# Kernel tuning notes

Measured on AMD Instinct MI355X. Metric: run time of the kernel, lower is better.

## Reference

```python
import jax, jax.numpy as jnp
import numpy as np

N, E = 50000, 800000
IN_DIM, HIDDEN, HEADS, OUT_DIM = 128, 64, 2, 128
NEG_SLOPE = 0.2


def setup_inputs() -> dict:
    key = jax.random.key(0)
    ks = jax.random.split(key, 12)
    s = lambda k, *sh: jax.random.normal(k, sh, dtype=jnp.float32) * (1.0 / np.sqrt(sh[0]))
    return {
        "x": jax.random.normal(ks[0], (N, IN_DIM), dtype=jnp.float32),
        "edge_index": jax.random.randint(ks[1], (2, E), 0, N, dtype=jnp.int64),
        # layer 1 (heads=2, concat=True)
        "Wl1": s(ks[2], IN_DIM, HEADS * HIDDEN),
        "Wr1": s(ks[3], IN_DIM, HEADS * HIDDEN),
        "att1": jax.random.normal(ks[4], (HEADS, HIDDEN), dtype=jnp.float32) * 0.1,
        "b1": jnp.zeros((HEADS * HIDDEN,), dtype=jnp.float32),
        # layer 2 (heads=1, concat=False -> mean)
        "Wl2": s(ks[5], HEADS * HIDDEN, OUT_DIM),
        "Wr2": s(ks[6], HEADS * HIDDEN, OUT_DIM),
        "att2": jax.random.normal(ks[7], (1, OUT_DIM), dtype=jnp.float32) * 0.1,
        "b2": jnp.zeros((OUT_DIM,), dtype=jnp.float32),
    }


def _gatv2_layer(x, src, dst, Wl, Wr, att, bias, heads, concat):
    n = x.shape[0]
    c = Wl.shape[1] // heads
    xl = (x @ Wl).reshape(n, heads, c)  # source transform
    xr = (x @ Wr).reshape(n, heads, c)  # target transform
    e = jax.nn.leaky_relu(xl[src] + xr[dst], NEG_SLOPE)      # (E, H, C)
    alpha = jnp.einsum("ehc,hc->eh", e, att)                 # (E, H)
    # softmax over incoming edges per destination node
    amax = jax.ops.segment_max(alpha, dst, num_segments=n)
    alpha = jnp.exp(alpha - amax[dst])
    denom = jax.ops.segment_sum(alpha, dst, num_segments=n)
    alpha = alpha / (denom[dst] + 1e-16)
    msg = xl[src] * alpha[:, :, None]                        # (E, H, C)
    out = jax.ops.segment_sum(msg, dst, num_segments=n)      # (N, H, C)
    out = out.reshape(n, heads * c) if concat else out.mean(axis=1)
    return out + bias


def reference(x, edge_index, Wl1, Wr1, att1, b1, Wl2, Wr2, att2, b2):
    n = x.shape[0]
    # PyG GATv2Conv default: add self loops
    loops = jnp.arange(n, dtype=edge_index.dtype)
    src = jnp.concatenate([edge_index[0], loops])
    dst = jnp.concatenate([edge_index[1], loops])
    h = jax.nn.elu(_gatv2_layer(x, src, dst, Wl1, Wr1, att1, b1, HEADS, True))
    h = jax.nn.elu(_gatv2_layer(h, src, dst, Wl2, Wr2, att2, b2, 1, False))
    return h
```

## Files before the change

### kernel.cpp

```cpp
#include <hip/hip_runtime.h>
#include <hip/hip_bf16.h>

#define N_NODES 50000
#define N_EDGES 800000
#define TOT_E   (N_EDGES + N_NODES)
#define NEG_SLOPE 0.2f
#define NBKT 196
#define NPB 256
#define BKT_CAP 6144
#define CHUNK 4096
#define NCHUNK ((TOT_E + CHUNK - 1) / CHUNK)

typedef __attribute__((ext_vector_type(8))) short bf16x8;
typedef __attribute__((ext_vector_type(4))) float f32x4;

static __device__ __forceinline__ unsigned short f2bf(float f) {
    unsigned int u = __float_as_uint(f);
    unsigned int r = (u + 0x7FFFu + ((u >> 16) & 1u)) >> 16;
    return (unsigned short)r;
}
static __device__ __forceinline__ float bf2f(unsigned short h) {
    return __uint_as_float(((unsigned int)h) << 16);
}
static __device__ __forceinline__ unsigned short f2h(float f) {
    _Float16 h = (_Float16)f;
    return __builtin_bit_cast(unsigned short, h);
}
static __device__ __forceinline__ float h2f(unsigned short u) {
    return (float)__builtin_bit_cast(_Float16, u);
}

__global__ __launch_bounds__(1024) void kA(const int* __restrict__ srcp,
                                           const int* __restrict__ dstp,
                                           int* __restrict__ bcount,
                                           unsigned* __restrict__ ebuf) {
    __shared__ int h[NBKT];
    __shared__ int lbase[NBKT];
    __shared__ int lcur[NBKT];
    __shared__ int sc[256];
    __shared__ unsigned stage[CHUNK];
    int t = threadIdx.x;
    if (t < NBKT) h[t] = 0;
    __syncthreads();
    int base = blockIdx.x * CHUNK;
    int nloc = min(CHUNK, TOT_E - base);
    for (int i = t; i < nloc; i += 1024) {
        int e = base + i;
        int d = (e < N_EDGES) ? dstp[e] : (e - N_EDGES);
        atomicAdd(&h[d >> 8], 1);
    }
    __syncthreads();
    if (t < NBKT) lbase[t] = h[t] ? atomicAdd(&bcount[t], h[t]) : 0;
    if (t < 256) sc[t] = (t < NBKT) ? h[t] : 0;
    __syncthreads();
    for (int off = 1; off < 256; off <<= 1) {
        int v = (t < 256 && t >= off) ? sc[t - off] : 0;
        __syncthreads();
        if (t < 256) sc[t] += v;
        __syncthreads();
    }
    if (t < NBKT) lcur[t] = sc[t] - h[t];
    __syncthreads();
    for (int i = t; i < nloc; i += 1024) {
        int e = base + i;
        int d = (e < N_EDGES) ? dstp[e] : (e - N_EDGES);
        int s = (e < N_EDGES) ? srcp[e] : (e - N_EDGES);
        int b = d >> 8;
        int p = atomicAdd(&lcur[b], 1);
        stage[p] = (unsigned)s | ((unsigned)(d & 255) << 16) | ((unsigned)b << 24);
    }
    __syncthreads();
    for (int i = t; i < nloc; i += 1024) {
        unsigned v = stage[i];
        int b = v >> 24;
        int pl = lbase[b] + (i - (lcur[b] - h[b]));
        if (pl < BKT_CAP) ebuf[(size_t)b * BKT_CAP + pl] = v & 0xFFFFFFu;
    }
}

__global__ void kScanB(const int* __restrict__ bcount, int* __restrict__ bbase) {
    __shared__ int s[256];
    int t = threadIdx.x;
    int own = (t < NBKT) ? bcount[t] : 0;
    s[t] = own;
    __syncthreads();
    for (int off = 1; off < 256; off <<= 1) {
        int v = (t >= off) ? s[t - off] : 0;
        __syncthreads();
        s[t] += v;
        __syncthreads();
    }
    if (t < NBKT) bbase[t] = s[t] - own;
    if (t == NBKT - 1) bbase[NBKT] = s[t];
}

__global__ __launch_bounds__(1024) void kB(const unsigned* __restrict__ ebuf,
                                           const int* __restrict__ bcount,
                                           const int* __restrict__ bbase,
                                           int* __restrict__ rowptr,
                                           int* __restrict__ esrc) {
    __shared__ int h[NPB];
    __shared__ int sc[NPB];
    __shared__ int st2[BKT_CAP];
    int b = blockIdx.x;
    int t = threadIdx.x;
    int gb = bbase[b];
    int cnt = min(bcount[b], BKT_CAP);
    const unsigned* eb = ebuf + (size_t)b * BKT_CAP;
    if (t < NPB) h[t] = 0;
    __syncthreads();
    for (int i = t; i < cnt; i += 1024)
        atomicAdd(&h[(eb[i] >> 16) & 255], 1);
    __syncthreads();
    if (t < NPB) sc[t] = h[t];
    __syncthreads();
    for (int off = 1; off < NPB; off <<= 1) {
        int v = (t < NPB && t >= off) ? sc[t - off] : 0;
        __syncthreads();
        if (t < NPB) sc[t] += v;
        __syncthreads();
    }
    if (t < NPB) h[t] = sc[t] - h[t];
    __syncthreads();
    int node0 = b << 8;
    if (t < NPB && node0 + t < N_NODES) rowptr[node0 + t] = gb + h[t];
    if (b == NBKT - 1 && t == 0) rowptr[N_NODES] = TOT_E;
    for (int i = t; i < cnt; i += 1024) {
        unsigned v = eb[i];
        int p = atomicAdd(&h[(v >> 16) & 255], 1);
        st2[p] = (int)(v & 0xFFFFu);
    }
    __syncthreads();
    for (int i = t; i < cnt; i += 1024) esrc[gb + i] = st2[i];
}

__global__ void k_pack2(const float* __restrict__ Wl1, const float* __restrict__ Wr1,
                        const float* __restrict__ Wl2, const float* __restrict__ Wr2,
                        unsigned short* __restrict__ Bp1, unsigned short* __restrict__ Bp2) {
    int gidx = blockIdx.x * 256 + threadIdx.x;
    int which = gidx >> 16;
    int idx = gidx & 65535;
    const float* Wa = which ? Wl2 : Wl1;
    const float* Wb = which ? Wr2 : Wr1;
    unsigned short* Bp = which ? Bp2 : Bp1;
    int j = idx & 7, lane = (idx >> 3) & 63, t = idx >> 9;
    int ks = t >> 4, ctg = t & 15;
    int k = (ks * 32 + (lane >> 4) * 8 + j) & 127;
    int n = ctg * 16 + (lane & 15);
    float v = (n < 128) ? Wa[k * 128 + n] : Wb[k * 128 + (n - 128)];
    Bp[idx] = f2bf(v);
}

template <bool F32IN>
__global__ __launch_bounds__(256) void k_mfma_lin(const void* __restrict__ Ain,
                                                  const unsigned short* __restrict__ Bp,
                                                  unsigned short* __restrict__ outA,
                                                  unsigned short* __restrict__ outB, int M) {
    __shared__ unsigned short lds_a[64][264];
    int tid = threadIdx.x;
    int n0 = blockIdx.x * 64;
    if (F32IN) {
        const float* X = (const float*)Ain;
#pragma unroll
        for (int r = 0; r < 8; ++r) {
            int c = r * 256 + tid;
            int row = c >> 5;
            int col4 = (c & 31) * 4;
            int gr = n0 + row;
            if (gr >= M) gr = M - 1;
            float4 v = *(const float4*)&X[(size_t)gr * 128 + col4];
            float vv[4] = {v.x, v.y, v.z, v.w};
            ushort4 hh, ll;
            unsigned short* hp = &hh.x;
            unsigned short* lp = &ll.x;
#pragma unroll
            for (int q = 0; q < 4; ++q) {
                unsigned short hv = f2bf(vv[q]);
                hp[q] = hv;
                lp[q] = f2bf(vv[q] - bf2f(hv));
            }
            *(ushort4*)&lds_a[row][col4] = hh;
            *(ushort4*)&lds_a[row][128 + col4] = ll;
        }
    } else {
        const unsigned short* Ap = (const unsigned short*)Ain;
#pragma unroll
        for (int r = 0; r < 8; ++r) {
            int c = r * 256 + tid;
            int row = c >> 5;
            int col = (c & 31) * 8;
            int gr = n0 + row;
            if (gr >= M) gr = M - 1;
            float4 v = *(const float4*)&Ap[(size_t)gr * 256 + col];
            *(float4*)&lds_a[row][col] = v;
        }
    }
    __syncthreads();

    int w = tid >> 6, lane = tid & 63;
    int lrow = lane & 15, lhi = lane >> 4;
    f32x4 acc[4][4] = {};
    const bf16x8* Bf = (const bf16x8*)Bp;
#pragma unroll
    for (int ks = 0; ks < 8; ++ks) {
        bf16x8 bfr[4], afr[4];
#pragma unroll
        for (int ct = 0; ct < 4; ++ct)
            bfr[ct] = Bf[(ks * 16 + (w * 4 + ct)) * 64 + lane];
#pragma unroll
        for (int mt = 0; mt < 4; ++mt)
            afr[mt] = *(const bf16x8*)&lds_a[mt * 16 + lrow][ks * 32 + lhi * 8];
#pragma unroll
        for (int mt = 0; mt < 4; ++mt)
#pragma unroll
            for (int ct = 0; ct < 4; ++ct)
                acc[mt][ct] = __builtin_amdgcn_mfma_f32_16x16x32_bf16(
                    afr[mt], bfr[ct], acc[mt][ct], 0, 0, 0);
    }
#pragma unroll
    for (int mt = 0; mt < 4; ++mt) {
        int row0 = n0 + mt * 16 + lhi * 4;
#pragma unroll
        for (int ct = 0; ct < 4; ++ct) {
            int col = w * 64 + ct * 16 + lrow;
            unsigned short* dst = (col < 128) ? outA : outB;
            int cc = col & 127;
#pragma unroll
            for (int reg = 0; reg < 4; ++reg) {
                int rg = row0 + reg;
                if (rg < M) dst[(size_t)rg * 128 + cc] = f2h(acc[mt][ct][reg]);
            }
        }
    }
}

template <int H, bool BF16OUT>
__global__ __launch_bounds__(256) void k_gat(const int* __restrict__ rowptr,
                                             const int* __restrict__ esrc,
                                             const unsigned short* __restrict__ xlh,
                                             const unsigned short* __restrict__ xrh,
                                             const float* __restrict__ att,
                                             const float* __restrict__ bias,
                                             float* __restrict__ out,
                                             unsigned short* __restrict__ outb) {
    int n = (blockIdx.x * 256 + threadIdx.x) >> 6;
    int lane = threadIdx.x & 63;
    if (n >= N_NODES) return;
    int start = rowptr[n], end = rowptr[n + 1];
    int grp = lane >> 4, sub = lane & 15;
    int c0 = sub * 8;

    float xr8[8], a8[8];
    {
        uint4 u = *(const uint4*)&xrh[(size_t)n * 128 + c0];
        unsigned int uu[4] = {u.x, u.y, u.z, u.w};
#pragma unroll
        for (int q = 0; q < 4; ++q) {
            xr8[2 * q]     = h2f((unsigned short)uu[q]);
            xr8[2 * q + 1] = h2f((unsigned short)(uu[q] >> 16));
        }
        float4 av0 = *(const float4*)&att[c0];
        float4 av1 = *(const float4*)&att[c0 + 4];
        a8[0] = av0.x; a8[1] = av0.y; a8[2] = av0.z; a8[3] = av0.w;
        a8[4] = av1.x; a8[5] = av1.y; a8[6] = av1.z; a8[7] = av1.w;
    }

    float m = -1e30f, den = 0.f;
    float acc[8] = {0.f, 0.f, 0.f, 0.f, 0.f, 0.f, 0.f, 0.f};

    int last = end - 1;
    auto cidx = [&](int e) { return esrc[(e < end) ? e : last]; };
    int sA = cidx(start + grp);
    int sB = cidx(start + 4 + grp);
    int sC = cidx(start + 8 + grp);
    uint4 u0 = *(const uint4*)&xlh[(size_t)sA * 128 + c0];
    uint4 u1 = *(const uint4*)&xlh[(size_t)sB * 128 + c0];

    for (int i = start; i < end; i += 4) {
        bool valid = (i + grp) < end;
        uint4 uc = u0;
        u0 = u1;
        u1 = *(const uint4*)&xlh[(size_t)sC * 128 + c0];
        sC = cidx(i + 12 + grp);
        unsigned int uu[4] = {uc.x, uc.y, uc.z, uc.w};
        float c[8];
#pragma unroll
        for (int q = 0; q < 4; ++q) {
            c[2 * q]     = h2f((unsigned short)uu[q]);
            c[2 * q + 1] = h2f((unsigned short)(uu[q] >> 16));
        }
        float t = 0.f;
#pragma unroll
        for (int j = 0; j < 8; ++j) {
            float v = c[j] + xr8[j];
            v = fmaxf(v, NEG_SLOPE * v);
            t = fmaf(v, a8[j], t);
        }
        const int STEPS = (H == 2) ? 3 : 4;
#pragma unroll
        for (int k = 0; k < STEPS; ++k)
            t += __shfl_xor(t, 1 << k, 64);
        float sc = valid ? t : -1e38f;

        float mn = fmaxf(m, sc);
        float corr = __expf(m - mn);
        float p = __expf(sc - mn);
        m = mn;
        den = fmaf(den, corr, p);
#pragma unroll
        for (int j = 0; j < 8; ++j)
            acc[j] = fmaf(acc[j], corr, p * c[j]);
    }

#pragma unroll
    for (int off = 16; off <= 32; off <<= 1) {
        float mo = __shfl_xor(m, off, 64);
        float deno = __shfl_xor(den, off, 64);
        float ao[8];
#pragma unroll
        for (int j = 0; j < 8; ++j) ao[j] = __shfl_xor(acc[j], off, 64);
        float mn = fmaxf(m, mo);
        float c1 = __expf(m - mn);
        float c2 = __expf(mo - mn);
        m = mn;
        den = den * c1 + deno * c2;
#pragma unroll
        for (int j = 0; j < 8; ++j)
            acc[j] = fmaf(acc[j], c1, ao[j] * c2);
    }

    if (grp == 0) {
        float inv = 1.f / (den + 1e-16f);
        float o[8];
        float4 bv0 = *(const float4*)&bias[c0];
        float4 bv1 = *(const float4*)&bias[c0 + 4];
        float bb[8] = {bv0.x, bv0.y, bv0.z, bv0.w, bv1.x, bv1.y, bv1.z, bv1.w};
#pragma unroll
        for (int j = 0; j < 8; ++j) {
            float v = fmaf(acc[j], inv, bb[j]);
            o[j] = (v > 0.f) ? v : (__expf(v) - 1.f);
        }
        if (BF16OUT) {
            unsigned short hi[8], lo[8];
#pragma unroll
            for (int j = 0; j < 8; ++j) {
                hi[j] = f2bf(o[j]);
                lo[j] = f2bf(o[j] - bf2f(hi[j]));
            }
            *(uint4*)&outb[(size_t)n * 256 + c0] = *(const uint4*)hi;
            *(uint4*)&outb[(size_t)n * 256 + 128 + c0] = *(const uint4*)lo;
        } else {
            *(float4*)&out[(size_t)n * 128 + c0] = make_float4(o[0], o[1], o[2], o[3]);
            *(float4*)&out[(size_t)n * 128 + c0 + 4] = make_float4(o[4], o[5], o[6], o[7]);
        }
    }
}

extern "C" void kernel_launch(void* const* d_in, const int* in_sizes, int n_in,
                              void* d_out, int out_size, void* d_ws, size_t ws_size,
                              hipStream_t stream) {
    const float* x    = (const float*)d_in[0];
    const int*   ei   = (const int*)d_in[1];
    const float* Wl1  = (const float*)d_in[2];
    const float* Wr1  = (const float*)d_in[3];
    const float* att1 = (const float*)d_in[4];
    const float* b1   = (const float*)d_in[5];
    const float* Wl2  = (const float*)d_in[6];
    const float* Wr2  = (const float*)d_in[7];
    const float* att2 = (const float*)d_in[8];
    const float* b2   = (const float*)d_in[9];
    const int* srcp = ei;
    const int* dstp = ei + N_EDGES;

    char* ws = (char*)d_ws;
    size_t off = 0;
    auto alloc = [&](size_t bytes) {
        void* p = ws + off;
        off = (off + bytes + 255) & ~(size_t)255;
        return p;
    };
    int*      bcount  = (int*)alloc(NBKT * sizeof(int));
    int*      bbase   = (int*)alloc((NBKT + 1) * sizeof(int));
    unsigned* ebuf    = (unsigned*)alloc((size_t)NBKT * BKT_CAP * sizeof(unsigned));
    int*      rowptr  = (int*)alloc((N_NODES + 1) * sizeof(int));
    int*      esrc    = (int*)alloc((size_t)TOT_E * sizeof(int));
    unsigned short* xp  = (unsigned short*)alloc((size_t)N_NODES * 256 * sizeof(short));
    unsigned short* Bp1 = (unsigned short*)alloc(65536 * sizeof(short));
    unsigned short* Bp2 = (unsigned short*)alloc(65536 * sizeof(short));
    unsigned short* xl  = (unsigned short*)alloc((size_t)N_NODES * 128 * sizeof(short));
    unsigned short* xr  = (unsigned short*)alloc((size_t)N_NODES * 128 * sizeof(short));

    hipMemsetAsync(bcount, 0, NBKT * sizeof(int), stream);
    kA<<<NCHUNK, 1024, 0, stream>>>(srcp, dstp, bcount, ebuf);
    kScanB<<<1, 256, 0, stream>>>(bcount, bbase);
    kB<<<NBKT, 1024, 0, stream>>>(ebuf, bcount, bbase, rowptr, esrc);

    k_pack2<<<512, 256, 0, stream>>>(Wl1, Wr1, Wl2, Wr2, Bp1, Bp2);

    int mfma_grid = (N_NODES + 63) / 64;

    k_mfma_lin<true><<<mfma_grid, 256, 0, stream>>>(x, Bp1, xl, xr, N_NODES);
    k_gat<2, true><<<(N_NODES + 3) / 4, 256, 0, stream>>>(rowptr, esrc, xl, xr, att1, b1,
                                                          nullptr, xp);
    k_mfma_lin<false><<<mfma_grid, 256, 0, stream>>>(xp, Bp2, xl, xr, N_NODES);
    k_gat<1, false><<<(N_NODES + 3) / 4, 256, 0, stream>>>(rowptr, esrc, xl, xr, att2, b2,
                                                           (float*)d_out, nullptr);
}
```

Before: 166.8 us.

## Fuse layer-1 GEMM with edge bucketing and fold the bucket scan into the CSR build

Layer-1 MFMA GEMM blocks and edge-bucketing blocks now run in one launch, branching on block index, so the two independent stages can overlap. The separate bucket-base scan kernel is merged into the per-bucket CSR kernel, which now recomputes the 196-entry prefix in every block. The bcount memset is replaced by zeroing inside the weight-pack kernel, and the bucketing kernels drop from 1024 to 256 threads. Nontemporal loads are added for streaming reads, trading fewer launches and more overlap for redundant scan work and a mixed-role grid that shares one shared-memory allocation sized for the GEMM.

```diff
diff --git a/kernel.cpp b/kernel.cpp
--- a/kernel.cpp
+++ b/kernel.cpp
@@ -10,9 +10,11 @@
 #define BKT_CAP 6144
 #define CHUNK 4096
 #define NCHUNK ((TOT_E + CHUNK - 1) / CHUNK)
+#define GEMM_BLKS ((N_NODES + 63) / 64)
 
 typedef __attribute__((ext_vector_type(8))) short bf16x8;
 typedef __attribute__((ext_vector_type(4))) float f32x4;
+typedef __attribute__((ext_vector_type(4))) unsigned int u32x4;
 
 static __device__ __forceinline__ unsigned short f2bf(float f) {
     unsigned int u = __float_as_uint(f);
@@ -30,113 +32,214 @@
     return (float)__builtin_bit_cast(_Float16, u);
 }
 
-__global__ __launch_bounds__(1024) void kA(const int* __restrict__ srcp,
-                                           const int* __restrict__ dstp,
-                                           int* __restrict__ bcount,
-                                           unsigned* __restrict__ ebuf) {
-    __shared__ int h[NBKT];
-    __shared__ int lbase[NBKT];
-    __shared__ int lcur[NBKT];
-    __shared__ int sc[256];
-    __shared__ unsigned stage[CHUNK];
+struct SmemGemm { unsigned short lds_a[64][264]; };
+struct SmemKA {
+    int h[NBKT];
+    int lbase[NBKT];
+    int lcur[NBKT];
+    int sc[256];
+    unsigned stage[CHUNK];
+};
+
+static __device__ void kA_body(SmemKA* s, int blk, const int* __restrict__ srcp,
+                               const int* __restrict__ dstp, int* __restrict__ bcount,
+                               unsigned* __restrict__ ebuf) {
     int t = threadIdx.x;
-    if (t < NBKT) h[t] = 0;
-    __syncthreads();
-    int base = blockIdx.x * CHUNK;
+    if (t < NBKT) s->h[t] = 0;
+    __syncthreads();
+    int base = blk * CHUNK;
     int nloc = min(CHUNK, TOT_E - base);
-    for (int i = t; i < nloc; i += 1024) {
+    for (int i = t; i < nloc; i += 256) {
         int e = base + i;
         int d = (e < N_EDGES) ? dstp[e] : (e - N_EDGES);
-        atomicAdd(&h[d >> 8], 1);
-    }
-    __syncthreads();
-    if (t < NBKT) lbase[t] = h[t] ? atomicAdd(&bcount[t], h[t]) : 0;
-    if (t < 256) sc[t] = (t < NBKT) ? h[t] : 0;
+        atomicAdd(&s->h[d >> 8], 1);
+    }
+    __syncthreads();
+    if (t < NBKT) s->lbase[t] = s->h[t] ? atomicAdd(&bcount[t], s->h[t]) : 0;
+    s->sc[t] = (t < NBKT) ? s->h[t] : 0;
     __syncthreads();
     for (int off = 1; off < 256; off <<= 1) {
-        int v = (t < 256 && t >= off) ? sc[t - off] : 0;
-        __syncthreads();
-        if (t < 256) sc[t] += v;
-        __syncthreads();
-    }
-    if (t < NBKT) lcur[t] = sc[t] - h[t];
-    __syncthreads();
-    for (int i = t; i < nloc; i += 1024) {
+        int v = (t >= off) ? s->sc[t - off] : 0;
+        __syncthreads();
+        s->sc[t] += v;
+        __syncthreads();
+    }
+    if (t < NBKT) s->lcur[t] = s->sc[t] - s->h[t];
+    __syncthreads();
+    for (int i = t; i < nloc; i += 256) {
         int e = base + i;
         int d = (e < N_EDGES) ? dstp[e] : (e - N_EDGES);
-        int s = (e < N_EDGES) ? srcp[e] : (e - N_EDGES);
+        int sv = (e < N_EDGES) ? srcp[e] : (e - N_EDGES);
         int b = d >> 8;
-        int p = atomicAdd(&lcur[b], 1);
-        stage[p] = (unsigned)s | ((unsigned)(d & 255) << 16) | ((unsigned)b << 24);
-    }
-    __syncthreads();
-    for (int i = t; i < nloc; i += 1024) {
-        unsigned v = stage[i];
+        int p = atomicAdd(&s->lcur[b], 1);
+        s->stage[p] = (unsigned)sv | ((unsigned)(d & 255) << 16) | ((unsigned)b << 24);
+    }
+    __syncthreads();
+    for (int i = t; i < nloc; i += 256) {
+        unsigned v = s->stage[i];
         int b = v >> 24;
-        int pl = lbase[b] + (i - (lcur[b] - h[b]));
+        int pl = s->lbase[b] + (i - (s->lcur[b] - s->h[b]));
         if (pl < BKT_CAP) ebuf[(size_t)b * BKT_CAP + pl] = v & 0xFFFFFFu;
     }
 }
 
-__global__ void kScanB(const int* __restrict__ bcount, int* __restrict__ bbase) {
-    __shared__ int s[256];
-    int t = threadIdx.x;
-    int own = (t < NBKT) ? bcount[t] : 0;
-    s[t] = own;
-    __syncthreads();
-    for (int off = 1; off < 256; off <<= 1) {
-        int v = (t >= off) ? s[t - off] : 0;
-        __syncthreads();
-        s[t] += v;
-        __syncthreads();
-    }
-    if (t < NBKT) bbase[t] = s[t] - own;
-    if (t == NBKT - 1) bbase[NBKT] = s[t];
-}
-
-__global__ __launch_bounds__(1024) void kB(const unsigned* __restrict__ ebuf,
+template <bool F32IN>
+static __device__ void gemm_body(SmemGemm* sg, int bid, const void* __restrict__ Ain,
+                                 const unsigned short* __restrict__ Bp,
+                                 unsigned short* __restrict__ outA,
+                                 unsigned short* __restrict__ outB, int M) {
+    int tid = threadIdx.x;
+    int n0 = bid * 64;
+    if (F32IN) {
+        const float* X = (const float*)Ain;
+#pragma unroll
+        for (int r = 0; r < 8; ++r) {
+            int c = r * 256 + tid;
+            int row = c >> 5;
+            int col4 = (c & 31) * 4;
+            int gr = n0 + row;
+            if (gr >= M) gr = M - 1;
+            f32x4 v = __builtin_nontemporal_load((const f32x4*)&X[(size_t)gr * 128 + col4]);
+            ushort4 hh, ll;
+            unsigned short* hp = &hh.x;
+            unsigned short* lp = &ll.x;
+#pragma unroll
+            for (int q = 0; q < 4; ++q) {
+                unsigned short hv = f2bf(v[q]);
+                hp[q] = hv;
+                lp[q] = f2bf(v[q] - bf2f(hv));
+            }
+            *(ushort4*)&sg->lds_a[row][col4] = hh;
+            *(ushort4*)&sg->lds_a[row][128 + col4] = ll;
+        }
+    } else {
+        const unsigned short* Ap = (const unsigned short*)Ain;
+#pragma unroll
+        for (int r = 0; r < 8; ++r) {
+            int c = r * 256 + tid;
+            int row = c >> 5;
+            int col = (c & 31) * 8;
+            int gr = n0 + row;
+            if (gr >= M) gr = M - 1;
+            u32x4 v = __builtin_nontemporal_load((const u32x4*)&Ap[(size_t)gr * 256 + col]);
+            *(u32x4*)&sg->lds_a[row][col] = v;
+        }
+    }
+    __syncthreads();
+
+    int w = tid >> 6, lane = tid & 63;
+    int lrow = lane & 15, lhi = lane >> 4;
+    f32x4 acc[4][4] = {};
+    const bf16x8* Bf = (const bf16x8*)Bp;
+#pragma unroll
+    for (int ks = 0; ks < 8; ++ks) {
+        bf16x8 bfr[4], afr[4];
+#pragma unroll
+        for (int ct = 0; ct < 4; ++ct)
+            bfr[ct] = Bf[(ks * 16 + (w * 4 + ct)) * 64 + lane];
+#pragma unroll
+        for (int mt = 0; mt < 4; ++mt)
+            afr[mt] = *(const bf16x8*)&sg->lds_a[mt * 16 + lrow][ks * 32 + lhi * 8];
+#pragma unroll
+        for (int mt = 0; mt < 4; ++mt)
+#pragma unroll
+            for (int ct = 0; ct < 4; ++ct)
+                acc[mt][ct] = __builtin_amdgcn_mfma_f32_16x16x32_bf16(
+                    afr[mt], bfr[ct], acc[mt][ct], 0, 0, 0);
+    }
+#pragma unroll
+    for (int mt = 0; mt < 4; ++mt) {
+        int row0 = n0 + mt * 16 + lhi * 4;
+#pragma unroll
+        for (int ct = 0; ct < 4; ++ct) {
+            int col = w * 64 + ct * 16 + lrow;
+            unsigned short* dst = (col < 128) ? outA : outB;
+            int cc = col & 127;
+#pragma unroll
+            for (int reg = 0; reg < 4; ++reg) {
+                int rg = row0 + reg;
+                if (rg < M) dst[(size_t)rg * 128 + cc] = f2h(acc[mt][ct][reg]);
+            }
+        }
+    }
+}
+
+__global__ __launch_bounds__(256) void k_fused1(const float* __restrict__ x,
+                                                const unsigned short* __restrict__ Bp1,
+                                                unsigned short* __restrict__ xl,
+                                                unsigned short* __restrict__ xr,
+                                                const int* __restrict__ srcp,
+                                                const int* __restrict__ dstp,
+                                                int* __restrict__ bcount,
+                                                unsigned* __restrict__ ebuf) {
+    __shared__ __align__(16) unsigned char smem[sizeof(SmemGemm)];
+    if (blockIdx.x < GEMM_BLKS)
+        gemm_body<true>((SmemGemm*)smem, blockIdx.x, x, Bp1, xl, xr, N_NODES);
+    else
+        kA_body((SmemKA*)smem, blockIdx.x - GEMM_BLKS, srcp, dstp, bcount, ebuf);
+}
+
+__global__ __launch_bounds__(256) void k_mfma_lin2(const unsigned short* __restrict__ Ap,
+                                                   const unsigned short* __restrict__ Bp,
+                                                   unsigned short* __restrict__ outA,
+                                                   unsigned short* __restrict__ outB, int M) {
+    __shared__ __align__(16) unsigned char smem[sizeof(SmemGemm)];
+    gemm_body<false>((SmemGemm*)smem, blockIdx.x, Ap, Bp, outA, outB, M);
+}
+
+__global__ __launch_bounds__(256) void kBs(const unsigned* __restrict__ ebuf,
                                            const int* __restrict__ bcount,
-                                           const int* __restrict__ bbase,
                                            int* __restrict__ rowptr,
                                            int* __restrict__ esrc) {
+    __shared__ int sall[256];
     __shared__ int h[NPB];
     __shared__ int sc[NPB];
     __shared__ int st2[BKT_CAP];
-    int b = blockIdx.x;
-    int t = threadIdx.x;
-    int gb = bbase[b];
+    int b = blockIdx.x, t = threadIdx.x;
+    int own = (t < NBKT) ? bcount[t] : 0;
+    sall[t] = own;
+    __syncthreads();
+    for (int off = 1; off < 256; off <<= 1) {
+        int v = (t >= off) ? sall[t - off] : 0;
+        __syncthreads();
+        sall[t] += v;
+        __syncthreads();
+    }
+    int gb = (b == 0) ? 0 : sall[b - 1];
     int cnt = min(bcount[b], BKT_CAP);
     const unsigned* eb = ebuf + (size_t)b * BKT_CAP;
-    if (t < NPB) h[t] = 0;
-    __syncthreads();
-    for (int i = t; i < cnt; i += 1024)
+    h[t] = 0;
+    __syncthreads();
+    for (int i = t; i < cnt; i += 256)
         atomicAdd(&h[(eb[i] >> 16) & 255], 1);
     __syncthreads();
-    if (t < NPB) sc[t] = h[t];
-    __syncthreads();
-    for (int off = 1; off < NPB; off <<= 1) {
-        int v = (t < NPB && t >= off) ? sc[t - off] : 0;
-        __syncthreads();
-        if (t < NPB) sc[t] += v;
-        __syncthreads();
-    }
-    if (t < NPB) h[t] = sc[t] - h[t];
+    sc[t] = h[t];
+    __syncthreads();
+    for (int off = 1; off < 256; off <<= 1) {
+        int v = (t >= off) ? sc[t - off] : 0;
+        __syncthreads();
+        sc[t] += v;
+        __syncthreads();
+    }
+    h[t] = sc[t] - h[t];
     __syncthreads();
     int node0 = b << 8;
-    if (t < NPB && node0 + t < N_NODES) rowptr[node0 + t] = gb + h[t];
+    if (node0 + t < N_NODES) rowptr[node0 + t] = gb + h[t];
     if (b == NBKT - 1 && t == 0) rowptr[N_NODES] = TOT_E;
-    for (int i = t; i < cnt; i += 1024) {
+    for (int i = t; i < cnt; i += 256) {
         unsigned v = eb[i];
         int p = atomicAdd(&h[(v >> 16) & 255], 1);
         st2[p] = (int)(v & 0xFFFFu);
     }
     __syncthreads();
-    for (int i = t; i < cnt; i += 1024) esrc[gb + i] = st2[i];
+    for (int i = t; i < cnt; i += 256) esrc[gb + i] = st2[i];
 }
 
 __global__ void k_pack2(const float* __restrict__ Wl1, const float* __restrict__ Wr1,
                         const float* __restrict__ Wl2, const float* __restrict__ Wr2,
-                        unsigned short* __restrict__ Bp1, unsigned short* __restrict__ Bp2) {
+                        unsigned short* __restrict__ Bp1, unsigned short* __restrict__ Bp2,
+                        int* __restrict__ bcount) {
+    if (blockIdx.x == 0 && threadIdx.x < NBKT) bcount[threadIdx.x] = 0;
     int gidx = blockIdx.x * 256 + threadIdx.x;
     int which = gidx >> 16;
     int idx = gidx & 65535;
@@ -149,89 +252,6 @@
     int n = ctg * 16 + (lane & 15);
     float v = (n < 128) ? Wa[k * 128 + n] : Wb[k * 128 + (n - 128)];
     Bp[idx] = f2bf(v);
-}
-
-template <bool F32IN>
-__global__ __launch_bounds__(256) void k_mfma_lin(const void* __restrict__ Ain,
-                                                  const unsigned short* __restrict__ Bp,
-                                                  unsigned short* __restrict__ outA,
-                                                  unsigned short* __restrict__ outB, int M) {
-    __shared__ unsigned short lds_a[64][264];
-    int tid = threadIdx.x;
-    int n0 = blockIdx.x * 64;
-    if (F32IN) {
-        const float* X = (const float*)Ain;
-#pragma unroll
-        for (int r = 0; r < 8; ++r) {
-            int c = r * 256 + tid;
-            int row = c >> 5;
-            int col4 = (c & 31) * 4;
-            int gr = n0 + row;
-            if (gr >= M) gr = M - 1;
-            float4 v = *(const float4*)&X[(size_t)gr * 128 + col4];
-            float vv[4] = {v.x, v.y, v.z, v.w};
-            ushort4 hh, ll;
-            unsigned short* hp = &hh.x;
-            unsigned short* lp = &ll.x;
-#pragma unroll
-            for (int q = 0; q < 4; ++q) {
-                unsigned short hv = f2bf(vv[q]);
-                hp[q] = hv;
-                lp[q] = f2bf(vv[q] - bf2f(hv));
-            }
-            *(ushort4*)&lds_a[row][col4] = hh;
-            *(ushort4*)&lds_a[row][128 + col4] = ll;
-        }
-    } else {
-        const unsigned short* Ap = (const unsigned short*)Ain;
-#pragma unroll
-        for (int r = 0; r < 8; ++r) {
-            int c = r * 256 + tid;
-            int row = c >> 5;
-            int col = (c & 31) * 8;
-            int gr = n0 + row;
-            if (gr >= M) gr = M - 1;
-            float4 v = *(const float4*)&Ap[(size_t)gr * 256 + col];
-            *(float4*)&lds_a[row][col] = v;
-        }
-    }
-    __syncthreads();
-
-    int w = tid >> 6, lane = tid & 63;
-    int lrow = lane & 15, lhi = lane >> 4;
-    f32x4 acc[4][4] = {};
-    const bf16x8* Bf = (const bf16x8*)Bp;
-#pragma unroll
-    for (int ks = 0; ks < 8; ++ks) {
-        bf16x8 bfr[4], afr[4];
-#pragma unroll
-        for (int ct = 0; ct < 4; ++ct)
-            bfr[ct] = Bf[(ks * 16 + (w * 4 + ct)) * 64 + lane];
-#pragma unroll
-        for (int mt = 0; mt < 4; ++mt)
-            afr[mt] = *(const bf16x8*)&lds_a[mt * 16 + lrow][ks * 32 + lhi * 8];
-#pragma unroll
-        for (int mt = 0; mt < 4; ++mt)
-#pragma unroll
-            for (int ct = 0; ct < 4; ++ct)
-                acc[mt][ct] = __builtin_amdgcn_mfma_f32_16x16x32_bf16(
-                    afr[mt], bfr[ct], acc[mt][ct], 0, 0, 0);
-    }
-#pragma unroll
-    for (int mt = 0; mt < 4; ++mt) {
-        int row0 = n0 + mt * 16 + lhi * 4;
-#pragma unroll
-        for (int ct = 0; ct < 4; ++ct) {
-            int col = w * 64 + ct * 16 + lrow;
-            unsigned short* dst = (col < 128) ? outA : outB;
-            int cc = col & 127;
-#pragma unroll
-            for (int reg = 0; reg < 4; ++reg) {
-                int rg = row0 + reg;
-                if (rg < M) dst[(size_t)rg * 128 + cc] = f2h(acc[mt][ct][reg]);
-            }
-        }
-    }
 }
 
 template <int H, bool BF16OUT>
@@ -252,12 +272,11 @@
 
     float xr8[8], a8[8];
     {
-        uint4 u = *(const uint4*)&xrh[(size_t)n * 128 + c0];
-        unsigned int uu[4] = {u.x, u.y, u.z, u.w};
+        u32x4 u = __builtin_nontemporal_load((const u32x4*)&xrh[(size_t)n * 128 + c0]);
 #pragma unroll
         for (int q = 0; q < 4; ++q) {
-            xr8[2 * q]     = h2f((unsigned short)uu[q]);
-            xr8[2 * q + 1] = h2f((unsigned short)(uu[q] >> 16));
+            xr8[2 * q]     = h2f((unsigned short)u[q]);
+            xr8[2 * q + 1] = h2f((unsigned short)(u[q] >> 16));
         }
         float4 av0 = *(const float4*)&att[c0];
         float4 av1 = *(const float4*)&att[c0 + 4];
@@ -269,25 +288,26 @@
     float acc[8] = {0.f, 0.f, 0.f, 0.f, 0.f, 0.f, 0.f, 0.f};
 
     int last = end - 1;
-    auto cidx = [&](int e) { return esrc[(e < end) ? e : last]; };
+    auto cidx = [&](int e) {
+        return __builtin_nontemporal_load(&esrc[(e < end) ? e : last]);
+    };
     int sA = cidx(start + grp);
     int sB = cidx(start + 4 + grp);
     int sC = cidx(start + 8 + grp);
-    uint4 u0 = *(const uint4*)&xlh[(size_t)sA * 128 + c0];
-    uint4 u1 = *(const uint4*)&xlh[(size_t)sB * 128 + c0];
+    u32x4 u0 = *(const u32x4*)&xlh[(size_t)sA * 128 + c0];
+    u32x4 u1 = *(const u32x4*)&xlh[(size_t)sB * 128 + c0];
 
     for (int i = start; i < end; i += 4) {
         bool valid = (i + grp) < end;
-        uint4 uc = u0;
+        u32x4 uc = u0;
         u0 = u1;
-        u1 = *(const uint4*)&xlh[(size_t)sC * 128 + c0];
+        u1 = *(const u32x4*)&xlh[(size_t)sC * 128 + c0];
         sC = cidx(i + 12 + grp);
-        unsigned int uu[4] = {uc.x, uc.y, uc.z, uc.w};
         float c[8];
 #pragma unroll
         for (int q = 0; q < 4; ++q) {
-            c[2 * q]     = h2f((unsigned short)uu[q]);
-            c[2 * q + 1] = h2f((unsigned short)(uu[q] >> 16));
+            c[2 * q]     = h2f((unsigned short)uc[q]);
+            c[2 * q + 1] = h2f((unsigned short)(uc[q] >> 16));
         }
         float t = 0.f;
 #pragma unroll
@@ -341,14 +361,17 @@
             o[j] = (v > 0.f) ? v : (__expf(v) - 1.f);
         }
         if (BF16OUT) {
-            unsigned short hi[8], lo[8];
-#pragma unroll
-            for (int j = 0; j < 8; ++j) {
-                hi[j] = f2bf(o[j]);
-                lo[j] = f2bf(o[j] - bf2f(hi[j]));
+            u32x4 hv, lv;
+#pragma unroll
+            for (int q = 0; q < 4; ++q) {
+                unsigned short h0 = f2bf(o[2 * q]), h1 = f2bf(o[2 * q + 1]);
+                unsigned short l0 = f2bf(o[2 * q] - bf2f(h0));
+                unsigned short l1 = f2bf(o[2 * q + 1] - bf2f(h1));
+                hv[q] = (unsigned)h0 | ((unsigned)h1 << 16);
+                lv[q] = (unsigned)l0 | ((unsigned)l1 << 16);
             }
-            *(uint4*)&outb[(size_t)n * 256 + c0] = *(const uint4*)hi;
-            *(uint4*)&outb[(size_t)n * 256 + 128 + c0] = *(const uint4*)lo;
+            *(u32x4*)&outb[(size_t)n * 256 + c0] = hv;
+            *(u32x4*)&outb[(size_t)n * 256 + 128 + c0] = lv;
         } else {
             *(float4*)&out[(size_t)n * 128 + c0] = make_float4(o[0], o[1], o[2], o[3]);
             *(float4*)&out[(size_t)n * 128 + c0 + 4] = make_float4(o[4], o[5], o[6], o[7]);
@@ -380,7 +403,6 @@
         return p;
     };
     int*      bcount  = (int*)alloc(NBKT * sizeof(int));
-    int*      bbase   = (int*)alloc((NBKT + 1) * sizeof(int));
     unsigned* ebuf    = (unsigned*)alloc((size_t)NBKT * BKT_CAP * sizeof(unsigned));
     int*      rowptr  = (int*)alloc((N_NODES + 1) * sizeof(int));
     int*      esrc    = (int*)alloc((size_t)TOT_E * sizeof(int));
@@ -390,19 +412,17 @@
     unsigned short* xl  = (unsigned short*)alloc((size_t)N_NODES * 128 * sizeof(short));
     unsigned short* xr  = (unsigned short*)alloc((size_t)N_NODES * 128 * sizeof(short));
 
-    hipMemsetAsync(bcount, 0, NBKT * sizeof(int), stream);
-    kA<<<NCHUNK, 1024, 0, stream>>>(srcp, dstp, bcount, ebuf);
-    kScanB<<<1, 256, 0, stream>>>(bcount, bbase);
-    kB<<<NBKT, 1024, 0, stream>>>(ebuf, bcount, bbase, rowptr, esrc);
-
-    k_pack2<<<512, 256, 0, stream>>>(Wl1, Wr1, Wl2, Wr2, Bp1, Bp2);
-
-    int mfma_grid = (N_NODES + 63) / 64;
-
-    k_mfma_lin<true><<<mfma_grid, 256, 0, stream>>>(x, Bp1, xl, xr, N_NODES);
+    k_pack2<<<512, 256, 0, stream>>>(Wl1, Wr1, Wl2, Wr2, Bp1, Bp2, bcount);
+
+    k_fused1<<<GEMM_BLKS + NCHUNK, 256, 0, stream>>>(x, Bp1, xl, xr, srcp, dstp,
+                                                     bcount, ebuf);
+
+    kBs<<<NBKT, 256, 0, stream>>>(ebuf, bcount, rowptr, esrc);
+
     k_gat<2, true><<<(N_NODES + 3) / 4, 256, 0, stream>>>(rowptr, esrc, xl, xr, att1, b1,
                                                           nullptr, xp);
-    k_mfma_lin<false><<<mfma_grid, 256, 0, stream>>>(xp, Bp2, xl, xr, N_NODES);
+    k_mfma_lin2<<<GEMM_BLKS, 256, 0, stream>>>(xp, Bp2, xl, xr, N_NODES);
+
     k_gat<1, false><<<(N_NODES + 3) / 4, 256, 0, stream>>>(rowptr, esrc, xl, xr, att2, b2,
                                                            (float*)d_out, nullptr);
 }
```

New measurement: 182.0 us. 9.1% more time.
